# Kernel tuning notes

Hardware: AMD Instinct MI355X
Metric: run time of the kernel (lower is better)

The kernel has to match this reference:

```python
import jax, jax.numpy as jnp
import numpy as np

N_NODES = 50000  # nodes in the (sub)graph


def setup_inputs() -> dict:
    key = jax.random.key(0)
    ks = jax.random.split(key, 8)
    nodes = jax.random.randint(ks[0], (N_NODES,), 0, 100000)
    src = jax.random.randint(ks[1], (800000,), 0, N_NODES)
    dst = jax.random.randint(ks[2], (800000,), 0, N_NODES)
    emb = jax.random.normal(ks[3], (100000, 256), dtype=jnp.float32)
    W = jax.random.normal(ks[4], (256, 128), dtype=jnp.float32) * 0.05
    b = jax.random.normal(ks[5], (128,), dtype=jnp.float32) * 0.05
    mlp_w = jax.random.normal(ks[6], (128, 40), dtype=jnp.float32) * 0.05
    mlp_b = jax.random.normal(ks[7], (40,), dtype=jnp.float32) * 0.05
    return {"nodes": nodes, "src": src, "dst": dst, "emb": emb,
            "W": W, "b": b, "mlp_w": mlp_w, "mlp_b": mlp_b}


def reference(nodes, src, dst, emb, W, b, mlp_w, mlp_b):
    n = N_NODES
    ones = jnp.ones_like(src, dtype=jnp.float32)
    out_deg = jax.ops.segment_sum(ones, src, num_segments=n)  # src out-degree
    in_deg = jax.ops.segment_sum(ones, dst, num_segments=n)   # dst in-degree
    norm_src = jax.lax.rsqrt(jnp.maximum(out_deg, 1.0))       # D_out^{-1/2}
    norm_dst = jax.lax.rsqrt(jnp.maximum(in_deg, 1.0))        # D_in^{-1/2}

    feat = emb[nodes]                                          # [N, in_dim]
    # dgl GraphConv(norm='both'): in_dim > out_dim -> project first, then aggregate
    h = (feat * norm_src[:, None]) @ W                         # [N, out_dim]
    agg = jax.ops.segment_sum(h[src], dst, num_segments=n)     # SpMM: sum over in-edges
    feat_out = agg * norm_dst[:, None] + b                     # [N, out_dim]

    logits = feat_out @ mlp_w + mlp_b                          # [N, num_classes]
    return (feat_out, logits)
```

## Files before the change

### kernel.cpp

```cpp
#include <hip/hip_runtime.h>

#define IN_DIM 256
#define OUT_DIM 128
#define N_CLS 40

#define SLICE 16384
#define NE_CH 40

typedef __attribute__((ext_vector_type(8))) short short8;
typedef __attribute__((ext_vector_type(4))) float floatx4;

static __device__ __forceinline__ unsigned short f2bf(float f) {
    union { float f; unsigned u; } v; v.f = f;
    unsigned r = v.u + 0x7FFF + ((v.u >> 16) & 1);
    return (unsigned short)(r >> 16);
}

__global__ __launch_bounds__(256) void hist_wconv_kernel(
    const int* __restrict__ src, const int* __restrict__ dst,
    int* __restrict__ partial_out, int* __restrict__ partial_in,
    const float* __restrict__ W, unsigned short* __restrict__ Wt,
    int ne, int n, int chunk, int nbh)
{
    __shared__ __align__(16) int lh_out[SLICE];
    __shared__ __align__(16) int lh_in[SLICE];

    const int tid = threadIdx.x;

    if (blockIdx.x >= nbh) {
        int t = (blockIdx.x - nbh) * 256 + tid;
        if (t < IN_DIM * OUT_DIM) {
            int k = t >> 7, c = t & 127;
            Wt[c * IN_DIM + k] = f2bf(W[t]);
        }
        return;
    }

    const int s = blockIdx.x / NE_CH;
    const int e = blockIdx.x % NE_CH;
    const int lo = s * SLICE;
    const int hi = min(lo + SLICE, n);

    for (int i = tid; i < SLICE; i += 256) { lh_out[i] = 0; lh_in[i] = 0; }
    __syncthreads();

    const int start = e * chunk;
    const int end = min(start + chunk, ne);
    const int cnt4 = (end - start) >> 2;
    const int4* s4 = (const int4*)(src + start);
    const int4* d4 = (const int4*)(dst + start);
    for (int k = tid; k < cnt4; k += 256) {
        int4 sv = s4[k];
        int4 dv = d4[k];
        unsigned q;
        q = (unsigned)(sv.x - lo); if (q < SLICE) atomicAdd(&lh_out[q], 1);
        q = (unsigned)(sv.y - lo); if (q < SLICE) atomicAdd(&lh_out[q], 1);
        q = (unsigned)(sv.z - lo); if (q < SLICE) atomicAdd(&lh_out[q], 1);
        q = (unsigned)(sv.w - lo); if (q < SLICE) atomicAdd(&lh_out[q], 1);
        q = (unsigned)(dv.x - lo); if (q < SLICE) atomicAdd(&lh_in[q], 1);
        q = (unsigned)(dv.y - lo); if (q < SLICE) atomicAdd(&lh_in[q], 1);
        q = (unsigned)(dv.z - lo); if (q < SLICE) atomicAdd(&lh_in[q], 1);
        q = (unsigned)(dv.w - lo); if (q < SLICE) atomicAdd(&lh_in[q], 1);
    }
    for (int t = start + (cnt4 << 2) + tid; t < end; t += 256) {
        unsigned q;
        q = (unsigned)(src[t] - lo); if (q < SLICE) atomicAdd(&lh_out[q], 1);
        q = (unsigned)(dst[t] - lo); if (q < SLICE) atomicAdd(&lh_in[q], 1);
    }
    __syncthreads();

    const int cnt = hi - lo;
    const int c4 = cnt >> 2;
    int4* po = (int4*)(partial_out + (size_t)e * n + lo);
    int4* pi = (int4*)(partial_in + (size_t)e * n + lo);
    for (int i = tid; i < c4; i += 256) {
        po[i] = ((const int4*)lh_out)[i];
        pi[i] = ((const int4*)lh_in)[i];
    }
    for (int i = (c4 << 2) + tid; i < cnt; i += 256) {
        partial_out[(size_t)e * n + lo + i] = lh_out[i];
        partial_in[(size_t)e * n + lo + i] = lh_in[i];
    }
}

__global__ __launch_bounds__(256) void reduce_kernel(
    int* __restrict__ partial_out, int* __restrict__ partial_in,
    int* __restrict__ cnt_out, int* __restrict__ cnt_in, int n)
{
    const int g = blockIdx.x * 256 + threadIdx.x;
    const int ng4 = n >> 2;
    if (g < ng4) {
        const size_t base = (size_t)g * 4;
        int4 sum = make_int4(0, 0, 0, 0);
#pragma unroll
        for (int e = 0; e < NE_CH; e++) {
            int4 v = *(const int4*)(partial_out + (size_t)e * n + base);
            sum.x += v.x; sum.y += v.y; sum.z += v.z; sum.w += v.w;
        }
        *(int4*)(cnt_out + base) = sum;

        int4 run = make_int4(0, 0, 0, 0);
#pragma unroll
        for (int e = 0; e < NE_CH; e++) {
            int* p = partial_in + (size_t)e * n + base;
            int4 v = *(const int4*)p;
            *(int4*)p = run;
            run.x += v.x; run.y += v.y; run.z += v.z; run.w += v.w;
        }
        *(int4*)(cnt_in + base) = run;
    }
    const int t = (ng4 << 2) + g;
    if (t < n) {
        int sum = 0;
#pragma unroll
        for (int e = 0; e < NE_CH; e++) sum += partial_out[(size_t)e * n + t];
        cnt_out[t] = sum;
        int run = 0;
#pragma unroll
        for (int e = 0; e < NE_CH; e++) {
            int v = partial_in[(size_t)e * n + t];
            partial_in[(size_t)e * n + t] = run;
            run += v;
        }
        cnt_in[t] = run;
    }
}

__global__ __launch_bounds__(1024) void scan_kernel(
    const int* __restrict__ cnt, int* __restrict__ row_start, int n)
{
    __shared__ int wsum[16];
    __shared__ int carry_s;
    const int tid = threadIdx.x;
    const int lane = tid & 63, wid = tid >> 6;
    if (tid == 0) carry_s = 0;
    __syncthreads();

    for (int chunk = 0; chunk < n; chunk += 8192) {
        int base = chunk + tid * 8;
        int v[8];
        if (base + 8 <= n) {
            int4 a = *(const int4*)&cnt[base];
            int4 b = *(const int4*)&cnt[base + 4];
            v[0]=a.x; v[1]=a.y; v[2]=a.z; v[3]=a.w;
            v[4]=b.x; v[5]=b.y; v[6]=b.z; v[7]=b.w;
        } else {
#pragma unroll
            for (int t = 0; t < 8; t++) v[t] = (base + t < n) ? cnt[base + t] : 0;
        }
        int tsum = 0;
#pragma unroll
        for (int t = 0; t < 8; t++) tsum += v[t];

        int incl = tsum;
#pragma unroll
        for (int off = 1; off < 64; off <<= 1) {
            int q = __shfl_up(incl, (unsigned)off, 64);
            if (lane >= off) incl += q;
        }
        if (lane == 63) wsum[wid] = incl;
        __syncthreads();
        int woff = 0;
        for (int w = 0; w < wid; ++w) woff += wsum[w];
        int carry = carry_s;
        int run = carry + woff + (incl - tsum);
        if (base + 8 <= n) {
            int o[8];
#pragma unroll
            for (int t = 0; t < 8; t++) { o[t] = run; run += v[t]; }
            int4 r0, r1;
            r0.x=o[0]; r0.y=o[1]; r0.z=o[2]; r0.w=o[3];
            r1.x=o[4]; r1.y=o[5]; r1.z=o[6]; r1.w=o[7];
            *(int4*)&row_start[base]     = r0;
            *(int4*)&row_start[base + 4] = r1;
        } else {
#pragma unroll
            for (int t = 0; t < 8; t++) {
                if (base + t < n) row_start[base + t] = run;
                run += v[t];
            }
        }
        __syncthreads();
        if (tid == 1023) carry_s = carry + woff + incl;
        __syncthreads();
    }
    if (tid == 0) row_start[n] = carry_s;
}

__global__ __launch_bounds__(256) void scatter_lds_kernel(
    const int* __restrict__ src, const int* __restrict__ dst,
    const int* __restrict__ row_start, const int* __restrict__ prefix_in,
    int* __restrict__ csr_src, int ne, int n, int chunk)
{
    __shared__ __align__(16) int cur[SLICE];

    const int tid = threadIdx.x;
    const int s = blockIdx.x / NE_CH;
    const int e = blockIdx.x % NE_CH;
    const int lo = s * SLICE;
    const int hi = min(lo + SLICE, n);
    const int cnt = hi - lo;

    const int c4 = cnt >> 2;
    for (int i = tid; i < c4; i += 256) {
        int4 rs = *(const int4*)(row_start + lo + i * 4);
        int4 pf = *(const int4*)(prefix_in + (size_t)e * n + lo + i * 4);
        rs.x += pf.x; rs.y += pf.y; rs.z += pf.z; rs.w += pf.w;
        ((int4*)cur)[i] = rs;
    }
    for (int i = (c4 << 2) + tid; i < cnt; i += 256)
        cur[i] = row_start[lo + i] + prefix_in[(size_t)e * n + lo + i];
    __syncthreads();

    const int start = e * chunk;
    const int end = min(start + chunk, ne);
    const int cnt4e = (end - start) >> 2;
    const int4* s4 = (const int4*)(src + start);
    const int4* d4 = (const int4*)(dst + start);
    for (int k = tid; k < cnt4e; k += 256) {
        int4 sv = s4[k];
        int4 dv = d4[k];
        unsigned q;
        q = (unsigned)(dv.x - lo); if (q < SLICE) csr_src[atomicAdd(&cur[q], 1)] = sv.x;
        q = (unsigned)(dv.y - lo); if (q < SLICE) csr_src[atomicAdd(&cur[q], 1)] = sv.y;
        q = (unsigned)(dv.z - lo); if (q < SLICE) csr_src[atomicAdd(&cur[q], 1)] = sv.z;
        q = (unsigned)(dv.w - lo); if (q < SLICE) csr_src[atomicAdd(&cur[q], 1)] = sv.w;
    }
    for (int t = start + (cnt4e << 2) + tid; t < end; t += 256) {
        unsigned q = (unsigned)(dst[t] - lo);
        if (q < SLICE) csr_src[atomicAdd(&cur[q], 1)] = src[t];
    }
}

__global__ __launch_bounds__(256) void gemm1_mfma_kernel(
    const int* __restrict__ nodes, const float* __restrict__ emb,
    const unsigned short* __restrict__ Wt, const int* __restrict__ cnt_out,
    unsigned short* __restrict__ h0, unsigned short* __restrict__ h1, int n)
{
    __shared__ unsigned short A_lds[128 * 40];
    __shared__ unsigned short B_lds[128 * 40];
    __shared__ int   snode[128];
    __shared__ float sscale[128];

    const int tid = threadIdx.x;
    const int m0  = blockIdx.x * 128;

    if (tid < 128) {
        int gr = m0 + tid;
        snode[tid]  = (gr < n) ? nodes[gr] : 0;
        sscale[tid] = (gr < n) ? rsqrtf(fmaxf((float)cnt_out[gr], 1.0f)) : 0.0f;
    }
    __syncthreads();

    const int arow = tid >> 1, aq = tid & 1;
    const float* aptr = emb + (size_t)snode[arow] * IN_DIM + aq * 16;
    const unsigned short* bptr = Wt + arow * IN_DIM + aq * 16;

    float    ar[16];
    unsigned bw[8];

#define LOAD_REGS(KK) do {                                           \
        _Pragma("unroll")                                            \
        for (int q = 0; q < 4; q++) {                                \
            const floatx4 v = *(const floatx4*)(aptr + (KK) * 32 + q * 4); \
            ar[q*4+0]=v[0]; ar[q*4+1]=v[1]; ar[q*4+2]=v[2]; ar[q*4+3]=v[3]; \
        }                                                            \
        const uint4 w0 = *(const uint4*)(bptr + (KK) * 32);          \
        const uint4 w1 = *(const uint4*)(bptr + (KK) * 32 + 8);      \
        bw[0]=w0.x; bw[1]=w0.y; bw[2]=w0.z; bw[3]=w0.w;              \
        bw[4]=w1.x; bw[5]=w1.y; bw[6]=w1.z; bw[7]=w1.w;              \
    } while (0)

#define WRITE_LDS() do {                                             \
        union { unsigned short s[16]; uint4 v[2]; } ua;              \
        _Pragma("unroll")                                            \
        for (int i = 0; i < 16; i++) ua.s[i] = f2bf(ar[i]);          \
        *(uint4*)&A_lds[arow * 40 + aq * 16]     = ua.v[0];          \
        *(uint4*)&A_lds[arow * 40 + aq * 16 + 8] = ua.v[1];          \
        uint4 b0, b1;                                                \
        b0.x=bw[0]; b0.y=bw[1]; b0.z=bw[2]; b0.w=bw[3];              \
        b1.x=bw[4]; b1.y=bw[5]; b1.z=bw[6]; b1.w=bw[7];              \
        *(uint4*)&B_lds[arow * 40 + aq * 16]     = b0;               \
        *(uint4*)&B_lds[arow * 40 + aq * 16 + 8] = b1;               \
    } while (0)

    const int wave = tid >> 6, lane = tid & 63;
    const int wr = (wave & 1) * 64;
    const int wc = (wave >> 1) * 64;
    const int fr = lane & 15;
    const int koff = (lane >> 4) * 8;

    floatx4 acc[4][4];
#pragma unroll
    for (int i = 0; i < 4; i++)
#pragma unroll
        for (int j = 0; j < 4; j++) acc[i][j] = (floatx4){0.f, 0.f, 0.f, 0.f};

    LOAD_REGS(0);
    WRITE_LDS();

    for (int kk = 0; kk < 8; ++kk) {
        if (kk < 7) LOAD_REGS(kk + 1);
        __syncthreads();
        short8 af[4], bf[4];
#pragma unroll
        for (int t = 0; t < 4; t++) {
            af[t] = *(const short8*)&A_lds[(wr + t * 16 + fr) * 40 + koff];
            bf[t] = *(const short8*)&B_lds[(wc + t * 16 + fr) * 40 + koff];
        }
#pragma unroll
        for (int rt = 0; rt < 4; rt++)
#pragma unroll
            for (int ct = 0; ct < 4; ct++)
                acc[rt][ct] = __builtin_amdgcn_mfma_f32_16x16x32_bf16(
                    bf[ct], af[rt], acc[rt][ct], 0, 0, 0);
        __syncthreads();
        if (kk < 7) WRITE_LDS();
    }

    unsigned short* hb = wc ? h1 : h0;
#pragma unroll
    for (int rt = 0; rt < 4; rt++) {
        int lrow = wr + rt * 16 + fr;
        int grow = m0 + lrow;
        float sc = sscale[lrow];
        if (grow < n) {
#pragma unroll
            for (int ct = 0; ct < 4; ct++) {
                int col = ct * 16 + (lane >> 4) * 4;
                union { unsigned short s[4]; uint2 v; } o;
                o.s[0] = f2bf(acc[rt][ct][0] * sc);
                o.s[1] = f2bf(acc[rt][ct][1] * sc);
                o.s[2] = f2bf(acc[rt][ct][2] * sc);
                o.s[3] = f2bf(acc[rt][ct][3] * sc);
                *(uint2*)&hb[(size_t)grow * 64 + col] = o.v;
            }
        }
    }
#undef LOAD_REGS
#undef WRITE_LDS
}

__global__ __launch_bounds__(256) void spmm_half_kernel(
    const int* __restrict__ row_start, const int* __restrict__ csr_src,
    const unsigned short* __restrict__ hh,
    const float* __restrict__ bias_half,
    float* __restrict__ out_col,
    int n)
{
    const int lane = threadIdx.x & 63;
    const int row = blockIdx.x * 4 + (threadIdx.x >> 6);
    if (row >= n) return;

    const int rs = row_start[row];
    const int re = row_start[row + 1];
    const int deg = re - rs;

    float a[4] = {0.f, 0.f, 0.f, 0.f};

    for (int base = 0; base < deg; base += 64) {
        const int cnt = min(deg - base, 64);
        int idx = (lane < cnt) ? csr_src[rs + base + lane] : 0;
        int t = 0;
        for (; t + 15 < cnt; t += 16) {
            int s[16];
#pragma unroll
            for (int u = 0; u < 16; u++) s[u] = __shfl(idx, t + u, 64);
            unsigned short v[16];
#pragma unroll
            for (int u = 0; u < 16; u++) v[u] = hh[(size_t)s[u] * 64 + lane];
#pragma unroll
            for (int u = 0; u < 16; u++) {
                union { unsigned uu; float f; } x;
                x.uu = ((unsigned)v[u]) << 16;
                a[u & 3] += x.f;
            }
        }
        for (; t + 3 < cnt; t += 4) {
            int s[4];
#pragma unroll
            for (int u = 0; u < 4; u++) s[u] = __shfl(idx, t + u, 64);
            unsigned short v[4];
#pragma unroll
            for (int u = 0; u < 4; u++) v[u] = hh[(size_t)s[u] * 64 + lane];
#pragma unroll
            for (int u = 0; u < 4; u++) {
                union { unsigned uu; float f; } x;
                x.uu = ((unsigned)v[u]) << 16;
                a[u] += x.f;
            }
        }
        for (; t < cnt; ++t) {
            int s0 = __shfl(idx, t, 64);
            union { unsigned uu; float f; } x;
            x.uu = ((unsigned)hh[(size_t)s0 * 64 + lane]) << 16;
            a[0] += x.f;
        }
    }

    const float nd = rsqrtf(fmaxf((float)deg, 1.0f));
    const float f0 = ((a[0] + a[1]) + (a[2] + a[3])) * nd + bias_half[lane];
    __builtin_nontemporal_store(f0, &out_col[(size_t)row * OUT_DIM + lane]);
}

__global__ __launch_bounds__(256) void mlp_mfma_kernel(
    const float* __restrict__ F, const float* __restrict__ mlp_w,
    const float* __restrict__ mlp_b, float* __restrict__ out_logits, int n)
{
    __shared__ unsigned short A_lds[48 * 136];
    __shared__ float s_mlpb[48];

    const int tid = threadIdx.x;
    for (int i = tid; i < 48 * 128; i += 256) {
        int cls = i >> 7, k = i & 127;
        A_lds[cls * 136 + k] =
            (cls < N_CLS) ? f2bf(mlp_w[(size_t)k * N_CLS + cls]) : (unsigned short)0;
    }
    if (tid < 48) s_mlpb[tid] = (tid < N_CLS) ? mlp_b[tid] : 0.f;
    __syncthreads();

    const int wave = tid >> 6, lane = tid & 63;
    const int r = lane & 15, koff = (lane >> 4) * 8;
    const int row = blockIdx.x * 64 + wave * 16 + r;
    const int rowc = (row < n) ? row : (n - 1);
    const float* fp = F + (size_t)rowc * OUT_DIM + koff;

    floatx4 acc[3];
#pragma unroll
    for (int ct = 0; ct < 3; ct++) acc[ct] = (floatx4){0.f, 0.f, 0.f, 0.f};

#pragma unroll
    for (int kk = 0; kk < 4; kk++) {
        floatx4 v0 = *(const floatx4*)(fp + kk * 32);
        floatx4 v1 = *(const floatx4*)(fp + kk * 32 + 4);
        union { unsigned short s[8]; short8 v; } bfr;
#pragma unroll
        for (int i = 0; i < 4; i++) {
            bfr.s[i]     = f2bf(v0[i]);
            bfr.s[4 + i] = f2bf(v1[i]);
        }
#pragma unroll
        for (int ct = 0; ct < 3; ct++) {
            short8 af = *(const short8*)&A_lds[(ct * 16 + r) * 136 + kk * 32 + koff];
            acc[ct] = __builtin_amdgcn_mfma_f32_16x16x32_bf16(af, bfr.v, acc[ct], 0, 0, 0);
        }
    }

    if (row < n) {
#pragma unroll
        for (int ct = 0; ct < 3; ct++)
#pragma unroll
            for (int i = 0; i < 4; i++) {
                int cls = ct * 16 + (lane >> 4) * 4 + i;
                if (cls < N_CLS)
                    __builtin_nontemporal_store(acc[ct][i] + s_mlpb[cls],
                        &out_logits[(size_t)row * N_CLS + cls]);
            }
    }
}

extern "C" void kernel_launch(void* const* d_in, const int* in_sizes, int n_in,
                              void* d_out, int out_size, void* d_ws, size_t ws_size,
                              hipStream_t stream) {
    const int*   nodes = (const int*)d_in[0];
    const int*   src   = (const int*)d_in[1];
    const int*   dst   = (const int*)d_in[2];
    const float* emb   = (const float*)d_in[3];
    const float* W     = (const float*)d_in[4];
    const float* b     = (const float*)d_in[5];
    const float* mlp_w = (const float*)d_in[6];
    const float* mlp_b = (const float*)d_in[7];

    const int n  = in_sizes[0];
    const int ne = in_sizes[1];

    int* cnt_out     = (int*)d_ws;
    int* cnt_in      = cnt_out + n;
    int* row_start   = cnt_in + n;
    int* csr_src     = row_start + n + 8;
    int* partial_out = csr_src + ne;
    int* partial_in  = partial_out + (size_t)NE_CH * n;
    size_t off = ((size_t)(3 * n + 8) + (size_t)ne + 2 * (size_t)NE_CH * n) * sizeof(int);
    off = (off + 15) & ~(size_t)15;
    unsigned short* Wt = (unsigned short*)((char*)d_ws + off);
    off += (size_t)IN_DIM * OUT_DIM * sizeof(unsigned short);
    off = (off + 15) & ~(size_t)15;
    unsigned short* h0 = (unsigned short*)((char*)d_ws + off);
    unsigned short* h1 = h0 + (size_t)n * 64;

    float* out_feat   = (float*)d_out;
    float* out_logits = out_feat + (size_t)n * OUT_DIM;

    const int ns = (n + SLICE - 1) / SLICE;
    const int chunk = (((ne + NE_CH - 1) / NE_CH) + 3) & ~3;
    const int nbh = ns * NE_CH;
    const int nbw = (IN_DIM * OUT_DIM + 255) / 256;

    hist_wconv_kernel<<<nbh + nbw, 256, 0, stream>>>(
        src, dst, partial_out, partial_in, W, Wt, ne, n, chunk, nbh);
    reduce_kernel<<<((n >> 2) + 255) / 256, 256, 0, stream>>>(
        partial_out, partial_in, cnt_out, cnt_in, n);
    scan_kernel<<<1, 1024, 0, stream>>>(cnt_in, row_start, n);
    scatter_lds_kernel<<<nbh, 256, 0, stream>>>(
        src, dst, row_start, partial_in, csr_src, ne, n, chunk);
    gemm1_mfma_kernel<<<(n + 127) / 128, 256, 0, stream>>>(
        nodes, emb, Wt, cnt_out, h0, h1, n);
    spmm_half_kernel<<<(n + 3) / 4, 256, 0, stream>>>(
        row_start, csr_src, h0, b, out_feat, n);
    spmm_half_kernel<<<(n + 3) / 4, 256, 0, stream>>>(
        row_start, csr_src, h1, b + 64, out_feat + 64, n);
    mlp_mfma_kernel<<<(n + 63) / 64, 256, 0, stream>>>(
        out_feat, mlp_w, mlp_b, out_logits, n);
}
```

Measured before the change: 152.6 us.

## Fuse degree reduce with block-local scan, add tiny block-offset scan, packed bf16 converts

Replaces the single-block 1024-thread serial scan over all nodes with a multi-block scan fused into the partial-histogram reduction. Each block writes local prefixes plus a block sum, and a one-wave kernel scans the block sums. Consumers (scatter and SpMM) add the block offset when they read row_start. Separately, software bf16 rounding is replaced with the hardware v_cvt_pk_bf16_f32 packed conversion in the GEMM and MLP kernels. The goal is to remove the serialized scan launch and cut conversion ALU work, at the cost of an extra offset load in the consumers.

```diff
diff --git a/kernel.cpp b/kernel.cpp
--- a/kernel.cpp
+++ b/kernel.cpp
@@ -14,6 +14,12 @@
     union { float f; unsigned u; } v; v.f = f;
     unsigned r = v.u + 0x7FFF + ((v.u >> 16) & 1);
     return (unsigned short)(r >> 16);
+}
+
+static __device__ __forceinline__ unsigned cvtpk(float lo, float hi) {
+    unsigned r;
+    asm("v_cvt_pk_bf16_f32 %0, %1, %2" : "=v"(r) : "v"(lo), "v"(hi));
+    return r;
 }
 
 __global__ __launch_bounds__(256) void hist_wconv_kernel(
@@ -83,14 +89,19 @@
     }
 }
 
-__global__ __launch_bounds__(256) void reduce_kernel(
+__global__ __launch_bounds__(256) void reduce_scan_kernel(
     int* __restrict__ partial_out, int* __restrict__ partial_in,
-    int* __restrict__ cnt_out, int* __restrict__ cnt_in, int n)
-{
-    const int g = blockIdx.x * 256 + threadIdx.x;
-    const int ng4 = n >> 2;
-    if (g < ng4) {
-        const size_t base = (size_t)g * 4;
+    int* __restrict__ cnt_out, int* __restrict__ row_start,
+    int* __restrict__ bsum, int n)
+{
+    __shared__ int wsum[4];
+    const int tid = threadIdx.x;
+    const int lane = tid & 63, wid = tid >> 6;
+    const int base = blockIdx.x * 1024 + tid * 4;
+
+    int4 run = make_int4(0, 0, 0, 0);
+
+    if (base + 4 <= n) {
         int4 sum = make_int4(0, 0, 0, 0);
 #pragma unroll
         for (int e = 0; e < NE_CH; e++) {
@@ -99,7 +110,6 @@
         }
         *(int4*)(cnt_out + base) = sum;
 
-        int4 run = make_int4(0, 0, 0, 0);
 #pragma unroll
         for (int e = 0; e < NE_CH; e++) {
             int* p = partial_in + (size_t)e * n + base;
@@ -107,89 +117,79 @@
             *(int4*)p = run;
             run.x += v.x; run.y += v.y; run.z += v.z; run.w += v.w;
         }
-        *(int4*)(cnt_in + base) = run;
-    }
-    const int t = (ng4 << 2) + g;
-    if (t < n) {
-        int sum = 0;
-#pragma unroll
-        for (int e = 0; e < NE_CH; e++) sum += partial_out[(size_t)e * n + t];
-        cnt_out[t] = sum;
-        int run = 0;
-#pragma unroll
-        for (int e = 0; e < NE_CH; e++) {
-            int v = partial_in[(size_t)e * n + t];
-            partial_in[(size_t)e * n + t] = run;
-            run += v;
-        }
-        cnt_in[t] = run;
-    }
-}
-
-__global__ __launch_bounds__(1024) void scan_kernel(
-    const int* __restrict__ cnt, int* __restrict__ row_start, int n)
-{
-    __shared__ int wsum[16];
-    __shared__ int carry_s;
-    const int tid = threadIdx.x;
-    const int lane = tid & 63, wid = tid >> 6;
-    if (tid == 0) carry_s = 0;
+    } else if (base <= n) {
+        int rr[4] = {0, 0, 0, 0};
+#pragma unroll
+        for (int j = 0; j < 4; j++) {
+            int pos = base + j;
+            if (pos < n) {
+                int sum = 0, r = 0;
+                for (int e = 0; e < NE_CH; e++) {
+                    sum += partial_out[(size_t)e * n + pos];
+                    int v = partial_in[(size_t)e * n + pos];
+                    partial_in[(size_t)e * n + pos] = r;
+                    r += v;
+                }
+                cnt_out[pos] = sum;
+                rr[j] = r;
+            }
+        }
+        run.x = rr[0]; run.y = rr[1]; run.z = rr[2]; run.w = rr[3];
+    }
+
+    const int s = run.x + run.y + run.z + run.w;
+    const int e1 = run.x, e2 = run.x + run.y, e3 = run.x + run.y + run.z;
+
+    int incl = s;
+#pragma unroll
+    for (int off = 1; off < 64; off <<= 1) {
+        int q = __shfl_up(incl, (unsigned)off, 64);
+        if (lane >= off) incl += q;
+    }
+    if (lane == 63) wsum[wid] = incl;
     __syncthreads();
-
-    for (int chunk = 0; chunk < n; chunk += 8192) {
-        int base = chunk + tid * 8;
-        int v[8];
-        if (base + 8 <= n) {
-            int4 a = *(const int4*)&cnt[base];
-            int4 b = *(const int4*)&cnt[base + 4];
-            v[0]=a.x; v[1]=a.y; v[2]=a.z; v[3]=a.w;
-            v[4]=b.x; v[5]=b.y; v[6]=b.z; v[7]=b.w;
-        } else {
-#pragma unroll
-            for (int t = 0; t < 8; t++) v[t] = (base + t < n) ? cnt[base + t] : 0;
-        }
-        int tsum = 0;
-#pragma unroll
-        for (int t = 0; t < 8; t++) tsum += v[t];
-
-        int incl = tsum;
+    int woff = 0;
+    for (int w = 0; w < wid; ++w) woff += wsum[w];
+    const int texcl = woff + incl - s;
+
+    if (base + 4 <= n) {
+        int4 o = make_int4(texcl, texcl + e1, texcl + e2, texcl + e3);
+        *(int4*)(row_start + base) = o;
+    } else if (base <= n) {
+        const int eo[4] = {0, e1, e2, e3};
+#pragma unroll
+        for (int j = 0; j < 4; j++) {
+            int pos = base + j;
+            if (pos <= n) row_start[pos] = texcl + eo[j];
+        }
+    }
+    if (tid == 0) bsum[blockIdx.x] = wsum[0] + wsum[1] + wsum[2] + wsum[3];
+}
+
+__global__ __launch_bounds__(64) void scan2_kernel(
+    const int* __restrict__ bsum, int* __restrict__ boffs, int nb)
+{
+    const int lane = threadIdx.x & 63;
+    int carry = 0;
+    for (int c = 0; c < nb; c += 64) {
+        int i = c + lane;
+        int v = (i < nb) ? bsum[i] : 0;
+        int incl = v;
 #pragma unroll
         for (int off = 1; off < 64; off <<= 1) {
             int q = __shfl_up(incl, (unsigned)off, 64);
             if (lane >= off) incl += q;
         }
-        if (lane == 63) wsum[wid] = incl;
-        __syncthreads();
-        int woff = 0;
-        for (int w = 0; w < wid; ++w) woff += wsum[w];
-        int carry = carry_s;
-        int run = carry + woff + (incl - tsum);
-        if (base + 8 <= n) {
-            int o[8];
-#pragma unroll
-            for (int t = 0; t < 8; t++) { o[t] = run; run += v[t]; }
-            int4 r0, r1;
-            r0.x=o[0]; r0.y=o[1]; r0.z=o[2]; r0.w=o[3];
-            r1.x=o[4]; r1.y=o[5]; r1.z=o[6]; r1.w=o[7];
-            *(int4*)&row_start[base]     = r0;
-            *(int4*)&row_start[base + 4] = r1;
-        } else {
-#pragma unroll
-            for (int t = 0; t < 8; t++) {
-                if (base + t < n) row_start[base + t] = run;
-                run += v[t];
-            }
-        }
-        __syncthreads();
-        if (tid == 1023) carry_s = carry + woff + incl;
-        __syncthreads();
-    }
-    if (tid == 0) row_start[n] = carry_s;
+        if (i < nb) boffs[i] = carry + incl - v;
+        carry += __shfl(incl, 63, 64);
+    }
+    if (lane == 0) boffs[nb] = carry;
 }
 
 __global__ __launch_bounds__(256) void scatter_lds_kernel(
     const int* __restrict__ src, const int* __restrict__ dst,
-    const int* __restrict__ row_start, const int* __restrict__ prefix_in,
+    const int* __restrict__ row_start, const int* __restrict__ boffs,
+    const int* __restrict__ prefix_in,
     int* __restrict__ csr_src, int ne, int n, int chunk)
 {
     __shared__ __align__(16) int cur[SLICE];
@@ -203,13 +203,19 @@
 
     const int c4 = cnt >> 2;
     for (int i = tid; i < c4; i += 256) {
-        int4 rs = *(const int4*)(row_start + lo + i * 4);
-        int4 pf = *(const int4*)(prefix_in + (size_t)e * n + lo + i * 4);
-        rs.x += pf.x; rs.y += pf.y; rs.z += pf.z; rs.w += pf.w;
+        int idx4 = lo + i * 4;
+        int4 rs = *(const int4*)(row_start + idx4);
+        int4 pf = *(const int4*)(prefix_in + (size_t)e * n + idx4);
+        const int bo = boffs[idx4 >> 10];
+        rs.x += pf.x + bo; rs.y += pf.y + bo;
+        rs.z += pf.z + bo; rs.w += pf.w + bo;
         ((int4*)cur)[i] = rs;
     }
-    for (int i = (c4 << 2) + tid; i < cnt; i += 256)
-        cur[i] = row_start[lo + i] + prefix_in[(size_t)e * n + lo + i];
+    for (int i = (c4 << 2) + tid; i < cnt; i += 256) {
+        int pos = lo + i;
+        cur[i] = row_start[pos] + boffs[pos >> 10]
+               + prefix_in[(size_t)e * n + pos];
+    }
     __syncthreads();
 
     const int start = e * chunk;
@@ -272,11 +278,13 @@
     } while (0)
 
 #define WRITE_LDS() do {                                             \
-        union { unsigned short s[16]; uint4 v[2]; } ua;              \
-        _Pragma("unroll")                                            \
-        for (int i = 0; i < 16; i++) ua.s[i] = f2bf(ar[i]);          \
-        *(uint4*)&A_lds[arow * 40 + aq * 16]     = ua.v[0];          \
-        *(uint4*)&A_lds[arow * 40 + aq * 16 + 8] = ua.v[1];          \
+        uint4 uv0, uv1;                                              \
+        uv0.x = cvtpk(ar[0],  ar[1]);  uv0.y = cvtpk(ar[2],  ar[3]); \
+        uv0.z = cvtpk(ar[4],  ar[5]);  uv0.w = cvtpk(ar[6],  ar[7]); \
+        uv1.x = cvtpk(ar[8],  ar[9]);  uv1.y = cvtpk(ar[10], ar[11]);\
+        uv1.z = cvtpk(ar[12], ar[13]); uv1.w = cvtpk(ar[14], ar[15]);\
+        *(uint4*)&A_lds[arow * 40 + aq * 16]     = uv0;              \
+        *(uint4*)&A_lds[arow * 40 + aq * 16 + 8] = uv1;              \
         uint4 b0, b1;                                                \
         b0.x=bw[0]; b0.y=bw[1]; b0.z=bw[2]; b0.w=bw[3];              \
         b1.x=bw[4]; b1.y=bw[5]; b1.z=bw[6]; b1.w=bw[7];              \
@@ -328,12 +336,10 @@
 #pragma unroll
             for (int ct = 0; ct < 4; ct++) {
                 int col = ct * 16 + (lane >> 4) * 4;
-                union { unsigned short s[4]; uint2 v; } o;
-                o.s[0] = f2bf(acc[rt][ct][0] * sc);
-                o.s[1] = f2bf(acc[rt][ct][1] * sc);
-                o.s[2] = f2bf(acc[rt][ct][2] * sc);
-                o.s[3] = f2bf(acc[rt][ct][3] * sc);
-                *(uint2*)&hb[(size_t)grow * 64 + col] = o.v;
+                uint2 o;
+                o.x = cvtpk(acc[rt][ct][0] * sc, acc[rt][ct][1] * sc);
+                o.y = cvtpk(acc[rt][ct][2] * sc, acc[rt][ct][3] * sc);
+                *(uint2*)&hb[(size_t)grow * 64 + col] = o;
             }
         }
     }
@@ -342,7 +348,8 @@
 }
 
 __global__ __launch_bounds__(256) void spmm_half_kernel(
-    const int* __restrict__ row_start, const int* __restrict__ csr_src,
+    const int* __restrict__ row_start, const int* __restrict__ boffs,
+    const int* __restrict__ csr_src,
     const unsigned short* __restrict__ hh,
     const float* __restrict__ bias_half,
     float* __restrict__ out_col,
@@ -352,8 +359,8 @@
     const int row = blockIdx.x * 4 + (threadIdx.x >> 6);
     if (row >= n) return;
 
-    const int rs = row_start[row];
-    const int re = row_start[row + 1];
+    const int rs = row_start[row]     + boffs[row >> 10];
+    const int re = row_start[row + 1] + boffs[(row + 1) >> 10];
     const int deg = re - rs;
 
     float a[4] = {0.f, 0.f, 0.f, 0.f};
@@ -433,12 +440,11 @@
     for (int kk = 0; kk < 4; kk++) {
         floatx4 v0 = *(const floatx4*)(fp + kk * 32);
         floatx4 v1 = *(const floatx4*)(fp + kk * 32 + 4);
-        union { unsigned short s[8]; short8 v; } bfr;
-#pragma unroll
-        for (int i = 0; i < 4; i++) {
-            bfr.s[i]     = f2bf(v0[i]);
-            bfr.s[4 + i] = f2bf(v1[i]);
-        }
+        union { unsigned u32[4]; short8 v; } bfr;
+        bfr.u32[0] = cvtpk(v0[0], v0[1]);
+        bfr.u32[1] = cvtpk(v0[2], v0[3]);
+        bfr.u32[2] = cvtpk(v1[0], v1[1]);
+        bfr.u32[3] = cvtpk(v1[2], v1[3]);
 #pragma unroll
         for (int ct = 0; ct < 3; ct++) {
             short8 af = *(const short8*)&A_lds[(ct * 16 + r) * 136 + kk * 32 + koff];
@@ -475,8 +481,9 @@
     const int ne = in_sizes[1];
 
     int* cnt_out     = (int*)d_ws;
-    int* cnt_in      = cnt_out + n;
-    int* row_start   = cnt_in + n;
+    int* bsum        = cnt_out + n;
+    int* boffs       = bsum + 1024;
+    int* row_start   = cnt_out + 2 * n;
     int* csr_src     = row_start + n + 8;
     int* partial_out = csr_src + ne;
     int* partial_in  = partial_out + (size_t)NE_CH * n;
@@ -495,20 +502,21 @@
     const int chunk = (((ne + NE_CH - 1) / NE_CH) + 3) & ~3;
     const int nbh = ns * NE_CH;
     const int nbw = (IN_DIM * OUT_DIM + 255) / 256;
+    const int nb = (n + 1023) / 1024;
 
     hist_wconv_kernel<<<nbh + nbw, 256, 0, stream>>>(
         src, dst, partial_out, partial_in, W, Wt, ne, n, chunk, nbh);
-    reduce_kernel<<<((n >> 2) + 255) / 256, 256, 0, stream>>>(
-        partial_out, partial_in, cnt_out, cnt_in, n);
-    scan_kernel<<<1, 1024, 0, stream>>>(cnt_in, row_start, n);
+    reduce_scan_kernel<<<nb, 256, 0, stream>>>(
+        partial_out, partial_in, cnt_out, row_start, bsum, n);
+    scan2_kernel<<<1, 64, 0, stream>>>(bsum, boffs, nb);
     scatter_lds_kernel<<<nbh, 256, 0, stream>>>(
-        src, dst, row_start, partial_in, csr_src, ne, n, chunk);
+        src, dst, row_start, boffs, partial_in, csr_src, ne, n, chunk);
     gemm1_mfma_kernel<<<(n + 127) / 128, 256, 0, stream>>>(
         nodes, emb, Wt, cnt_out, h0, h1, n);
     spmm_half_kernel<<<(n + 3) / 4, 256, 0, stream>>>(
-        row_start, csr_src, h0, b, out_feat, n);
+        row_start, boffs, csr_src, h0, b, out_feat, n);
     spmm_half_kernel<<<(n + 3) / 4, 256, 0, stream>>>(
-        row_start, csr_src, h1, b + 64, out_feat + 64, n);
+        row_start, boffs, csr_src, h1, b + 64, out_feat + 64, n);
     mlp_mfma_kernel<<<(n + 63) / 64, 256, 0, stream>>>(
         out_feat, mlp_w, mlp_b, out_logits, n);
 }
```

After: 146.2 us. 4.2% less time.
